# Kernel optimization log

Measured on AMD Instinct MI355X. Metric: run time of the kernel, lower is better.

The kernel has to match this reference:

```python
import jax, jax.numpy as jnp
import numpy as np

N, E = 50000, 800000
IN, EIN, HID, OUT = 128, 64, 256, 256
L, H = 3, 4
D = HID // H  # per-head out_feats


def setup_inputs() -> dict:
    key = jax.random.key(0)
    ks = jax.random.split(key, 20)
    s = 0.02
    return {
        "h": jax.random.normal(ks[0], (N, IN), jnp.float32),
        "efeat": jax.random.normal(ks[1], (E, EIN), jnp.float32),
        "src": jax.random.randint(ks[2], (E,), 0, N, jnp.int32),
        "dst": jax.random.randint(ks[3], (E,), 0, N, jnp.int32),
        "enc_w": jax.random.normal(ks[4], (IN, HID), jnp.float32) * s,
        "enc_b": jnp.zeros((HID,), jnp.float32),
        "eenc_w": jax.random.normal(ks[5], (EIN, HID), jnp.float32) * s,
        "eenc_b": jnp.zeros((HID,), jnp.float32),
        "Wn": jax.random.normal(ks[6], (L, HID, HID), jnp.float32) * s,
        "We": jax.random.normal(ks[7], (L, HID, HID), jnp.float32) * s,
        "al": jax.random.normal(ks[8], (L, H, D), jnp.float32) * s,
        "ar": jax.random.normal(ks[9], (L, H, D), jnp.float32) * s,
        "ae": jax.random.normal(ks[10], (L, H, D), jnp.float32) * s,
        "ln_g": jnp.ones((L, HID), jnp.float32),
        "ln_b": jnp.zeros((L, HID), jnp.float32),
        "out_w": jax.random.normal(ks[11], (HID, OUT), jnp.float32) * s,
        "out_b": jnp.zeros((OUT,), jnp.float32),
    }


def reference(h, efeat, src, dst, enc_w, enc_b, eenc_w, eenc_b,
              Wn, We, al, ar, ae, ln_g, ln_b, out_w, out_b):
    # Dropout layers act as identity (eval mode).
    n = h.shape[0]
    x = h @ enc_w + enc_b                      # [N, HID] node encoder
    ef = efeat @ eenc_w + eenc_b               # [E, HID] edge encoder
    nl, nh, nd = al.shape
    for l in range(nl):
        res = x
        feat = (x @ Wn[l]).reshape(n, nh, nd)          # [N,H,D]
        eft = (ef @ We[l]).reshape(-1, nh, nd)         # [E,H,D]
        el = jnp.sum(feat * al[l], axis=-1)            # [N,H]
        er = jnp.sum(feat * ar[l], axis=-1)            # [N,H]
        ee = jnp.sum(eft * ae[l], axis=-1)             # [E,H]
        e = jax.nn.leaky_relu(el[src] + er[dst] + ee, 0.2)  # [E,H]
        # edge softmax over incoming edges of each dst node
        m = jax.lax.stop_gradient(jax.ops.segment_max(e, dst, num_segments=n))
        a = jnp.exp(e - m[dst])
        ssum = jax.ops.segment_sum(a, dst, num_segments=n)
        alpha = a / ssum[dst]                          # [E,H]
        agg = jax.ops.segment_sum(alpha[:, :, None] * feat[src], dst,
                                  num_segments=n)      # [N,H,D]
        x = jax.nn.relu(agg.reshape(n, nh * nd))
        y = x + res
        mu = jnp.mean(y, axis=-1, keepdims=True)
        var = jnp.var(y, axis=-1, keepdims=True)
        x = (y - mu) / jnp.sqrt(var + 1e-5) * ln_g[l] + ln_b[l]
    return x @ out_w + out_b
```

## Files before the change

### kernel.cpp

```cpp
#include <hip/hip_runtime.h>
#include <math.h>


typedef __attribute__((ext_vector_type(8))) short bf16x8;
typedef __attribute__((ext_vector_type(4))) float f32x4;

__device__ __forceinline__ ushort f2b(float f) {
    unsigned u; __builtin_memcpy(&u, &f, 4);
    unsigned r = u + 0x7FFF + ((u >> 16) & 1);
    return (ushort)(r >> 16);
}
__device__ __forceinline__ float b2f(ushort u) {
    unsigned x = (unsigned)u << 16;
    float f; __builtin_memcpy(&f, &x, 4);
    return f;
}

__global__ void k_deg(const int* __restrict__ dst, int* __restrict__ deg, int E) {
    int e = blockIdx.x * 256 + threadIdx.x;
    if (e < E) atomicAdd(&deg[dst[e]], 1);
}

__global__ void k_bsum(const int* __restrict__ deg, int* __restrict__ bsum, int n) {
    __shared__ int wsum[4];
    int tid = threadIdx.x;
    int idx = blockIdx.x * 1024 + tid * 4;
    int4 v = make_int4(0, 0, 0, 0);
    if (idx + 3 < n) v = *(const int4*)(deg + idx);
    else {
        if (idx + 0 < n) v.x = deg[idx + 0];
        if (idx + 1 < n) v.y = deg[idx + 1];
        if (idx + 2 < n) v.z = deg[idx + 2];
    }
    int s = v.x + v.y + v.z + v.w;
#pragma unroll
    for (int off = 32; off; off >>= 1) s += __shfl_down(s, off, 64);
    if ((tid & 63) == 0) wsum[tid >> 6] = s;
    __syncthreads();
    if (tid == 0) bsum[blockIdx.x] = wsum[0] + wsum[1] + wsum[2] + wsum[3];
}

__global__ void k_bscan(const int* __restrict__ bsum, int* __restrict__ boff,
                        int* __restrict__ rowp, int NB, int n) {
    int tid = threadIdx.x;
    int v = (tid < NB) ? bsum[tid] : 0;
    int sc = v;
#pragma unroll
    for (int off = 1; off < 64; off <<= 1) {
        int t = __shfl_up(sc, off, 64);
        if ((tid & 63) >= off) sc += t;
    }
    if (tid < NB) boff[tid] = sc - v;
    if (tid == 63) rowp[n] = sc;
}

__global__ void k_bwrite(const int* __restrict__ deg, const int* __restrict__ boff,
                         int* __restrict__ rowp, int* __restrict__ cursor, int n) {
    __shared__ int wsum[4];
    __shared__ int woff_sh[4];
    int tid = threadIdx.x;
    int lane = tid & 63, wid = tid >> 6;
    int idx = blockIdx.x * 1024 + tid * 4;
    int4 v = make_int4(0, 0, 0, 0);
    if (idx + 3 < n) v = *(const int4*)(deg + idx);
    else {
        if (idx + 0 < n) v.x = deg[idx + 0];
        if (idx + 1 < n) v.y = deg[idx + 1];
        if (idx + 2 < n) v.z = deg[idx + 2];
    }
    int sum4 = v.x + v.y + v.z + v.w;
    int sc = sum4;
#pragma unroll
    for (int off = 1; off < 64; off <<= 1) {
        int t = __shfl_up(sc, off, 64);
        if (lane >= off) sc += t;
    }
    if (lane == 63) wsum[wid] = sc;
    __syncthreads();
    if (tid < 4) {
        int o = 0;
        for (int w = 0; w < tid; w++) o += wsum[w];
        woff_sh[tid] = o;
    }
    __syncthreads();
    int ex = boff[blockIdx.x] + woff_sh[wid] + (sc - sum4);
    int p0 = ex, p1 = ex + v.x, p2 = p1 + v.y, p3 = p2 + v.z;
    if (idx + 0 < n) { rowp[idx + 0] = p0; cursor[idx + 0] = p0; }
    if (idx + 1 < n) { rowp[idx + 1] = p1; cursor[idx + 1] = p1; }
    if (idx + 2 < n) { rowp[idx + 2] = p2; cursor[idx + 2] = p2; }
    if (idx + 3 < n) { rowp[idx + 3] = p3; cursor[idx + 3] = p3; }
}

__global__ void k_scatter(const int* __restrict__ dst, const int* __restrict__ src,
                          int* __restrict__ cursor, int* __restrict__ eid,
                          int* __restrict__ esrc, int E) {
    int e = blockIdx.x * 256 + threadIdx.x;
    if (e < E) {
        int pos = atomicAdd(&cursor[dst[e]], 1);
        eid[pos] = e;
        esrc[pos] = src[e];
    }
}

__global__ void k_ew(const float* __restrict__ We, const float* __restrict__ ae,
                     float* __restrict__ ew) {
    int t = blockIdx.x * 256 + threadIdx.x;
    if (t >= 3072) return;
    int l = t >> 10, r = t & 1023;
    int k = r >> 2, h = r & 3;
    const float* w = We + (size_t)l * 65536 + (size_t)k * 256 + h * 64;
    const float* a = ae + l * 256 + h * 64;
    float s = 0.f;
    for (int d = 0; d < 64; d++) s += w[d] * a[d];
    ew[t] = s;
}

__global__ void k_eew(const float* __restrict__ eenc_w, const float* __restrict__ eenc_b,
                      const float* __restrict__ ew, float* __restrict__ eew2,
                      float* __restrict__ eeb) {
    int t = blockIdx.x * 256 + threadIdx.x;
    if (t < 768) {
        int j = t / 12, lh = t % 12;
        int l = lh >> 2, h = lh & 3;
        float s = 0.f;
        for (int k = 0; k < 256; k++) s += eenc_w[j * 256 + k] * ew[l * 1024 + k * 4 + h];
        eew2[j * 12 + lh] = s;
    } else if (t < 780) {
        int lh = t - 768;
        int l = lh >> 2, h = lh & 3;
        float s = 0.f;
        for (int k = 0; k < 256; k++) s += eenc_b[k] * ew[l * 1024 + k * 4 + h];
        eeb[lh] = s;
    }
}

__global__ __launch_bounds__(256) void k_ee(const float* __restrict__ efeat,
                                            const float* __restrict__ eew2,
                                            const float* __restrict__ eeb,
                                            const int* __restrict__ eid,
                                            float* __restrict__ ee_l,
                                            int E) {
    const int tid = threadIdx.x;
    const int lane = tid & 63;
    const int wave = tid >> 6;
    const int q = lane & 7;
    const int g8 = lane >> 3;

    float W[8][12];
#pragma unroll
    for (int u = 0; u < 4; u++)
#pragma unroll
        for (int t = 0; t < 12; t++) {
            W[u][t]     = eew2[(q * 4 + u) * 12 + t];
            W[u + 4][t] = eew2[(32 + q * 4 + u) * 12 + t];
        }
    float Bv[12];
#pragma unroll
    for (int t = 0; t < 12; t++) Bv[t] = eeb[t];

    const int base = blockIdx.x * 128 + wave * 32;
#pragma unroll
    for (int p = 0; p < 4; p++) {
        int pos = base + p * 8 + g8;
        if (pos >= E) return;
        int e = eid[pos];
        float4 v0 = *(const float4*)(efeat + (size_t)e * 64 + q * 4);
        float4 v1 = *(const float4*)(efeat + (size_t)e * 64 + 32 + q * 4);
        float acc[12];
#pragma unroll
        for (int t = 0; t < 12; t++)
            acc[t] = v0.x * W[0][t] + v0.y * W[1][t] + v0.z * W[2][t] + v0.w * W[3][t] +
                     v1.x * W[4][t] + v1.y * W[5][t] + v1.z * W[6][t] + v1.w * W[7][t];
#pragma unroll
        for (int m = 1; m < 8; m <<= 1)
#pragma unroll
            for (int t = 0; t < 12; t++) acc[t] += __shfl_xor(acc[t], m, 64);
        if (q == 0) {
#pragma unroll
            for (int l = 0; l < 3; l++) {
                float4 o = make_float4(acc[l * 4 + 0] + Bv[l * 4 + 0],
                                       acc[l * 4 + 1] + Bv[l * 4 + 1],
                                       acc[l * 4 + 2] + Bv[l * 4 + 2],
                                       acc[l * 4 + 3] + Bv[l * 4 + 3]);
                *(float4*)(ee_l + (size_t)l * E * 4 + (size_t)pos * 4) = o;
            }
        }
    }
}

__global__ void k_prep(const float* __restrict__ h, const float* __restrict__ enc_w,
                       const float* __restrict__ Wn, const float* __restrict__ out_w,
                       ushort* __restrict__ hb, ushort* __restrict__ encT,
                       ushort* __restrict__ WnT, ushort* __restrict__ outT, int n4) {
    int t = blockIdx.x * 256 + threadIdx.x;
    if (t < n4) {
        float4 v = *(const float4*)(h + (size_t)t * 4);
        ushort4 o;
        o.x = f2b(v.x); o.y = f2b(v.y); o.z = f2b(v.z); o.w = f2b(v.w);
        *(ushort4*)(hb + (size_t)t * 4) = o;
        return;
    }
    t -= n4;
    if (t < 32768) {
        int nn = t >> 7, k = t & 127;
        encT[t] = f2b(enc_w[k * 256 + nn]);
        return;
    }
    t -= 32768;
    if (t < 3 * 65536) {
        int l = t >> 16, r = t & 65535;
        int nn = r >> 8, k = r & 255;
        WnT[(size_t)l * 65536 + r] = f2b(Wn[(size_t)l * 65536 + k * 256 + nn]);
        return;
    }
    t -= 3 * 65536;
    if (t < 65536) {
        int nn = t >> 8, k = t & 255;
        outT[t] = f2b(out_w[k * 256 + nn]);
    }
}

template <int KTILES, bool BIAS, bool STORE_F32, bool STORE_BF16>
__global__ __launch_bounds__(256) void gemm_mfma(const ushort* __restrict__ A,
                                                 const ushort* __restrict__ BT,
                                                 const float* __restrict__ bias,
                                                 float* __restrict__ Cf,
                                                 ushort* __restrict__ Cb, int M) {
    constexpr int K = KTILES * 32;
    __shared__ __align__(16) ushort As[128 * 32];
    __shared__ __align__(16) ushort Bs[128 * 32];
    const int tid = threadIdx.x;
    const int wave = tid >> 6;
    const int lane = tid & 63;
    const int rowBase = blockIdx.x * 128;
    const int colBase = blockIdx.y * 128;
    const int sRow = lane >> 2;
    const int sCol = (lane & 3) * 8;
    const int c0 = wave * 2, c1 = wave * 2 + 1;

    const ushort* gA0 = A + (size_t)(rowBase + c0 * 16 + sRow) * K + sCol;
    const ushort* gA1 = A + (size_t)(rowBase + c1 * 16 + sRow) * K + sCol;
    const ushort* gB0 = BT + (size_t)(colBase + c0 * 16 + sRow) * K + sCol;
    const ushort* gB1 = BT + (size_t)(colBase + c1 * 16 + sRow) * K + sCol;
    ushort* lA0 = As + c0 * 512;
    ushort* lA1 = As + c1 * 512;
    ushort* lB0 = Bs + c0 * 512;
    ushort* lB1 = Bs + c1 * 512;

    f32x4 acc[4][4] = {};
    const int wr = (wave >> 1) * 64, wc = (wave & 1) * 64;
    const int ml = lane & 15, q = lane >> 4;

    for (int kt = 0; kt < KTILES; ++kt) {
        __builtin_amdgcn_global_load_lds(
            (const __attribute__((address_space(1))) unsigned*)(gA0 + kt * 32),
            (__attribute__((address_space(3))) unsigned*)lA0, 16, 0, 0);
        __builtin_amdgcn_global_load_lds(
            (const __attribute__((address_space(1))) unsigned*)(gA1 + kt * 32),
            (__attribute__((address_space(3))) unsigned*)lA1, 16, 0, 0);
        __builtin_amdgcn_global_load_lds(
            (const __attribute__((address_space(1))) unsigned*)(gB0 + kt * 32),
            (__attribute__((address_space(3))) unsigned*)lB0, 16, 0, 0);
        __builtin_amdgcn_global_load_lds(
            (const __attribute__((address_space(1))) unsigned*)(gB1 + kt * 32),
            (__attribute__((address_space(3))) unsigned*)lB1, 16, 0, 0);
        __syncthreads();
        bf16x8 af[4], bfr[4];
#pragma unroll
        for (int i = 0; i < 4; i++)
            af[i] = *(const bf16x8*)&As[(wr + i * 16 + ml) * 32 + q * 8];
#pragma unroll
        for (int j = 0; j < 4; j++)
            bfr[j] = *(const bf16x8*)&Bs[(wc + j * 16 + ml) * 32 + q * 8];
#pragma unroll
        for (int i = 0; i < 4; i++)
#pragma unroll
            for (int j = 0; j < 4; j++)
                acc[i][j] = __builtin_amdgcn_mfma_f32_16x16x32_bf16(af[i], bfr[j], acc[i][j],
                                                                    0, 0, 0);
        __syncthreads();
    }

#pragma unroll
    for (int j = 0; j < 4; j++) {
        const int col = colBase + wc + j * 16 + ml;
        const float bb = BIAS ? bias[col] : 0.f;
#pragma unroll
        for (int i = 0; i < 4; i++) {
#pragma unroll
            for (int r = 0; r < 4; r++) {
                const int row = rowBase + wr + i * 16 + q * 4 + r;
                if (row < M) {
                    float v = acc[i][j][r] + bb;
                    if (STORE_F32) Cf[(size_t)row * 256 + col] = v;
                    if (STORE_BF16) Cb[(size_t)row * 256 + col] = f2b(v);
                }
            }
        }
    }
}

__global__ __launch_bounds__(256) void k_elr(const ushort* __restrict__ feat,
                                             const float* __restrict__ al,
                                             const float* __restrict__ ar,
                                             float* __restrict__ el,
                                             float* __restrict__ er, int N) {
    int lane = threadIdx.x & 63;
    int n = blockIdx.x * 4 + (threadIdx.x >> 6);
    if (n >= N) return;
    ushort4 f4 = *(const ushort4*)&feat[(size_t)n * 256 + lane * 4];
    float4 a4 = *(const float4*)&al[lane * 4];
    float4 r4 = *(const float4*)&ar[lane * 4];
    float f0 = b2f(f4.x), f1 = b2f(f4.y), f2 = b2f(f4.z), f3 = b2f(f4.w);
    float va = f0 * a4.x + f1 * a4.y + f2 * a4.z + f3 * a4.w;
    float vr = f0 * r4.x + f1 * r4.y + f2 * r4.z + f3 * r4.w;
#pragma unroll
    for (int m = 1; m < 16; m <<= 1) {
        va += __shfl_xor(va, m, 64);
        vr += __shfl_xor(vr, m, 64);
    }
    if ((lane & 15) == 0) {
        int h = lane >> 4;
        el[n * 4 + h] = va;
        er[n * 4 + h] = vr;
    }
}

template <bool WRITE_X>
__global__ __launch_bounds__(256) void k_agg(const int* __restrict__ rowp,
                                             const int* __restrict__ esrc,
                                             const float* __restrict__ ee,
                                             const float* __restrict__ el,
                                             const float* __restrict__ er,
                                             const ushort* __restrict__ feat,
                                             float* __restrict__ x_io,
                                             ushort* __restrict__ xb,
                                             const float* __restrict__ g,
                                             const float* __restrict__ b, int N) {
    __shared__ float w_sh[4][64][4];
    __shared__ int s_sh[4][64];
    const int wv = threadIdx.x >> 6;
    const int lane = threadIdx.x & 63;
    const int n = blockIdx.x * 4 + wv;
    if (n >= N) return;
    const int start = rowp[n], end = rowp[n + 1];
    const int h = lane >> 4;

    float4 e4 = *(const float4*)(er + (size_t)n * 4);
    float ern[4] = {e4.x, e4.y, e4.z, e4.w};
    float wsum[4] = {0.f, 0.f, 0.f, 0.f};
    float acc[4] = {0.f, 0.f, 0.f, 0.f};

    for (int cs = start; cs < end; cs += 64) {
        const int m = min(64, end - cs);
        if (lane < m) {
            int pos = cs + lane;
            int s = esrc[pos];
            s_sh[wv][lane] = s;
            float4 eev = *(const float4*)(ee + (size_t)pos * 4);
            float4 elv = *(const float4*)(el + (size_t)s * 4);
            float ea[4] = {eev.x, eev.y, eev.z, eev.w};
            float la[4] = {elv.x, elv.y, elv.z, elv.w};
#pragma unroll
            for (int hh = 0; hh < 4; hh++) {
                float sc = la[hh] + ern[hh] + ea[hh];
                sc = (sc > 0.f) ? sc : 0.2f * sc;
                float w = __expf(sc);
                w_sh[wv][lane][hh] = w;
                wsum[hh] += w;
            }
        }
        asm volatile("s_waitcnt lgkmcnt(0)" ::: "memory");
        __builtin_amdgcn_sched_barrier(0);
        for (int j = 0; j < m; ++j) {
            int s = s_sh[wv][j];
            float w = w_sh[wv][j][h];
            ushort4 p = *(const ushort4*)&feat[(size_t)s * 256 + lane * 4];
            acc[0] += w * b2f(p.x);
            acc[1] += w * b2f(p.y);
            acc[2] += w * b2f(p.z);
            acc[3] += w * b2f(p.w);
        }
        asm volatile("s_waitcnt lgkmcnt(0)" ::: "memory");
        __builtin_amdgcn_sched_barrier(0);
    }

#pragma unroll
    for (int mm = 1; mm < 64; mm <<= 1)
#pragma unroll
        for (int hh = 0; hh < 4; hh++) wsum[hh] += __shfl_xor(wsum[hh], mm, 64);

    float inv = (end > start) ? 1.f / wsum[h] : 0.f;
    float4 xr = *(const float4*)&x_io[(size_t)n * 256 + lane * 4];
    float xra[4] = {xr.x, xr.y, xr.z, xr.w};
    float y[4];
    float s1 = 0.f, s2 = 0.f;
#pragma unroll
    for (int u = 0; u < 4; u++) {
        float v = fmaxf(acc[u] * inv, 0.f);
        y[u] = v + xra[u];
        s1 += y[u];
        s2 += y[u] * y[u];
    }
#pragma unroll
    for (int mm = 1; mm < 64; mm <<= 1) {
        s1 += __shfl_xor(s1, mm, 64);
        s2 += __shfl_xor(s2, mm, 64);
    }
    float mu = s1 * (1.f / 256.f);
    float var = s2 * (1.f / 256.f) - mu * mu;
    float rstd = rsqrtf(var + 1e-5f);
    float4 gv = *(const float4*)&g[lane * 4];
    float4 bv = *(const float4*)&b[lane * 4];
    float ga[4] = {gv.x, gv.y, gv.z, gv.w};
    float ba[4] = {bv.x, bv.y, bv.z, bv.w};
    float o[4];
    ushort4 ob;
#pragma unroll
    for (int u = 0; u < 4; u++) o[u] = (y[u] - mu) * rstd * ga[u] + ba[u];
    ob.x = f2b(o[0]); ob.y = f2b(o[1]); ob.z = f2b(o[2]); ob.w = f2b(o[3]);
    if (WRITE_X)
        *(float4*)&x_io[(size_t)n * 256 + lane * 4] = make_float4(o[0], o[1], o[2], o[3]);
    *(ushort4*)&xb[(size_t)n * 256 + lane * 4] = ob;
}

extern "C" void kernel_launch(void* const* d_in, const int* in_sizes, int n_in,
                              void* d_out, int out_size, void* d_ws, size_t ws_size,
                              hipStream_t stream) {
    const float* h      = (const float*)d_in[0];
    const float* efeat  = (const float*)d_in[1];
    const int*   src    = (const int*)d_in[2];
    const int*   dst    = (const int*)d_in[3];
    const float* enc_w  = (const float*)d_in[4];
    const float* enc_b  = (const float*)d_in[5];
    const float* eenc_w = (const float*)d_in[6];
    const float* eenc_b = (const float*)d_in[7];
    const float* Wn     = (const float*)d_in[8];
    const float* We     = (const float*)d_in[9];
    const float* al     = (const float*)d_in[10];
    const float* ar     = (const float*)d_in[11];
    const float* ae     = (const float*)d_in[12];
    const float* ln_g   = (const float*)d_in[13];
    const float* ln_b   = (const float*)d_in[14];
    const float* out_w  = (const float*)d_in[15];
    const float* out_b  = (const float*)d_in[16];

    const int N = in_sizes[0] / 128;
    const int E = in_sizes[2];
    const int Mpad = ((N + 127) / 128) * 128;
    const int NB = (N + 1023) / 1024;

    char* ws = (char*)d_ws;
    size_t off = 0;
    auto alloc = [&](size_t bytes) -> char* {
        char* p = ws + off;
        off += (bytes + 255) & ~(size_t)255;
        return p;
    };
    float*  X      = (float*)alloc((size_t)Mpad * 256 * 4);
    ushort* Xb     = (ushort*)alloc((size_t)Mpad * 256 * 2);
    ushort* F      = (ushort*)alloc((size_t)Mpad * 256 * 2);
    ushort* hb     = (ushort*)alloc((size_t)Mpad * 128 * 2);
    float*  el     = (float*)alloc((size_t)N * 4 * 4);
    float*  er     = (float*)alloc((size_t)N * 4 * 4);
    float*  ee_l   = (float*)alloc((size_t)E * 12 * 4);
    int*    esrc   = (int*)alloc((size_t)E * 4);
    int*    eid    = (int*)alloc((size_t)E * 4);
    int*    deg    = (int*)alloc((size_t)N * 4);
    int*    rowp   = (int*)alloc((size_t)(N + 1) * 4);
    int*    cursor = (int*)alloc((size_t)N * 4);
    int*    bsum   = (int*)alloc(64 * 4);
    int*    boff   = (int*)alloc(64 * 4);
    float*  ew     = (float*)alloc(3072 * 4);
    float*  eew2   = (float*)alloc(768 * 4);
    float*  eeb    = (float*)alloc(64);
    ushort* encT   = (ushort*)alloc(256 * 128 * 2);
    ushort* WnT    = (ushort*)alloc(3 * 256 * 256 * 2);
    ushort* outT   = (ushort*)alloc(256 * 256 * 2);
    (void)ws_size; (void)n_in; (void)out_size;

    hipMemsetAsync(deg, 0, (size_t)N * 4, stream);
    k_deg<<<(E + 255) / 256, 256, 0, stream>>>(dst, deg, E);
    k_bsum<<<NB, 256, 0, stream>>>(deg, bsum, N);
    k_bscan<<<1, 64, 0, stream>>>(bsum, boff, rowp, NB, N);
    k_bwrite<<<NB, 256, 0, stream>>>(deg, boff, rowp, cursor, N);
    k_scatter<<<(E + 255) / 256, 256, 0, stream>>>(dst, src, cursor, eid, esrc, E);

    k_ew<<<12, 256, 0, stream>>>(We, ae, ew);
    k_eew<<<4, 256, 0, stream>>>(eenc_w, eenc_b, ew, eew2, eeb);
    k_ee<<<(E + 127) / 128, 256, 0, stream>>>(efeat, eew2, eeb, eid, ee_l, E);

    const int n4 = N * 128 / 4;
    k_prep<<<(n4 + 32768 + 4 * 65536 + 255) / 256, 256, 0, stream>>>(
        h, enc_w, Wn, out_w, hb, encT, WnT, outT, n4);

    dim3 gG(Mpad / 128, 2);
    gemm_mfma<4, true, true, true><<<gG, 256, 0, stream>>>(hb, encT, enc_b, X, Xb, N);

    for (int l = 0; l < 3; l++) {
        gemm_mfma<8, false, false, true><<<gG, 256, 0, stream>>>(
            Xb, WnT + (size_t)l * 65536, nullptr, nullptr, F, N);
        k_elr<<<(N + 3) / 4, 256, 0, stream>>>(F, al + l * 256, ar + l * 256, el, er, N);
        if (l < 2)
            k_agg<true><<<(N + 3) / 4, 256, 0, stream>>>(rowp, esrc,
                ee_l + (size_t)l * E * 4, el, er, F, X, Xb, ln_g + l * 256,
                ln_b + l * 256, N);
        else
            k_agg<false><<<(N + 3) / 4, 256, 0, stream>>>(rowp, esrc,
                ee_l + (size_t)l * E * 4, el, er, F, X, Xb, ln_g + l * 256,
                ln_b + l * 256, N);
    }
    gemm_mfma<8, true, true, false><<<gG, 256, 0, stream>>>(Xb, outT, out_b,
                                                            (float*)d_out, nullptr, N);
}
```

Measured before the change: 862.5 us.

## Split edge gather across wave halves with 16-byte loads; drop fp32 residual copy

The aggregation kernel now has each half-wave process alternate edges and each lane load 8 bf16 features (16 bytes) instead of 4, combining the halves with a cross-half shuffle. The fp32 node-state buffer X is removed, so the residual is read from the bf16 copy Xb and only bf16 is written back. This cuts per-node global traffic and doubles in-flight gathers per lane. The residual path now carries bf16 rounding instead of fp32 precision, which may shift accuracy slightly.

```diff
diff --git a/kernel.cpp b/kernel.cpp
--- a/kernel.cpp
+++ b/kernel.cpp
@@ -3,6 +3,7 @@
 
 
 typedef __attribute__((ext_vector_type(8))) short bf16x8;
+typedef __attribute__((ext_vector_type(8))) unsigned short u16x8;
 typedef __attribute__((ext_vector_type(4))) float f32x4;
 
 __device__ __forceinline__ ushort f2b(float f) {
@@ -326,14 +327,12 @@
     }
 }
 
-template <bool WRITE_X>
 __global__ __launch_bounds__(256) void k_agg(const int* __restrict__ rowp,
                                              const int* __restrict__ esrc,
                                              const float* __restrict__ ee,
                                              const float* __restrict__ el,
                                              const float* __restrict__ er,
                                              const ushort* __restrict__ feat,
-                                             float* __restrict__ x_io,
                                              ushort* __restrict__ xb,
                                              const float* __restrict__ g,
                                              const float* __restrict__ b, int N) {
@@ -344,12 +343,14 @@
     const int n = blockIdx.x * 4 + wv;
     if (n >= N) return;
     const int start = rowp[n], end = rowp[n + 1];
-    const int h = lane >> 4;
+    const int half = lane >> 5;
+    const int c = lane & 31;
+    const int h = c >> 3;
 
     float4 e4 = *(const float4*)(er + (size_t)n * 4);
     float ern[4] = {e4.x, e4.y, e4.z, e4.w};
     float wsum[4] = {0.f, 0.f, 0.f, 0.f};
-    float acc[4] = {0.f, 0.f, 0.f, 0.f};
+    float acc[8] = {0.f, 0.f, 0.f, 0.f, 0.f, 0.f, 0.f, 0.f};
 
     for (int cs = start; cs < end; cs += 64) {
         const int m = min(64, end - cs);
@@ -372,33 +373,33 @@
         }
         asm volatile("s_waitcnt lgkmcnt(0)" ::: "memory");
         __builtin_amdgcn_sched_barrier(0);
-        for (int j = 0; j < m; ++j) {
+        for (int j = half; j < m; j += 2) {
             int s = s_sh[wv][j];
             float w = w_sh[wv][j][h];
-            ushort4 p = *(const ushort4*)&feat[(size_t)s * 256 + lane * 4];
-            acc[0] += w * b2f(p.x);
-            acc[1] += w * b2f(p.y);
-            acc[2] += w * b2f(p.z);
-            acc[3] += w * b2f(p.w);
+            u16x8 p = *(const u16x8*)&feat[(size_t)s * 256 + c * 8];
+#pragma unroll
+            for (int u = 0; u < 8; u++) acc[u] += w * b2f((ushort)p[u]);
         }
         asm volatile("s_waitcnt lgkmcnt(0)" ::: "memory");
         __builtin_amdgcn_sched_barrier(0);
     }
 
 #pragma unroll
+    for (int u = 0; u < 8; u++) acc[u] += __shfl_xor(acc[u], 32, 64);
+
+#pragma unroll
     for (int mm = 1; mm < 64; mm <<= 1)
 #pragma unroll
         for (int hh = 0; hh < 4; hh++) wsum[hh] += __shfl_xor(wsum[hh], mm, 64);
 
     float inv = (end > start) ? 1.f / wsum[h] : 0.f;
-    float4 xr = *(const float4*)&x_io[(size_t)n * 256 + lane * 4];
-    float xra[4] = {xr.x, xr.y, xr.z, xr.w};
-    float y[4];
+    u16x8 xr = *(const u16x8*)&xb[(size_t)n * 256 + c * 8];
+    float y[8];
     float s1 = 0.f, s2 = 0.f;
 #pragma unroll
-    for (int u = 0; u < 4; u++) {
+    for (int u = 0; u < 8; u++) {
         float v = fmaxf(acc[u] * inv, 0.f);
-        y[u] = v + xra[u];
+        y[u] = v + b2f((ushort)xr[u]);
         s1 += y[u];
         s2 += y[u] * y[u];
     }
@@ -407,21 +408,20 @@
         s1 += __shfl_xor(s1, mm, 64);
         s2 += __shfl_xor(s2, mm, 64);
     }
-    float mu = s1 * (1.f / 256.f);
-    float var = s2 * (1.f / 256.f) - mu * mu;
+    float mu = s1 * (1.f / 512.f);
+    float var = s2 * (1.f / 512.f) - mu * mu;
     float rstd = rsqrtf(var + 1e-5f);
-    float4 gv = *(const float4*)&g[lane * 4];
-    float4 bv = *(const float4*)&b[lane * 4];
-    float ga[4] = {gv.x, gv.y, gv.z, gv.w};
-    float ba[4] = {bv.x, bv.y, bv.z, bv.w};
-    float o[4];
-    ushort4 ob;
-#pragma unroll
-    for (int u = 0; u < 4; u++) o[u] = (y[u] - mu) * rstd * ga[u] + ba[u];
-    ob.x = f2b(o[0]); ob.y = f2b(o[1]); ob.z = f2b(o[2]); ob.w = f2b(o[3]);
-    if (WRITE_X)
-        *(float4*)&x_io[(size_t)n * 256 + lane * 4] = make_float4(o[0], o[1], o[2], o[3]);
-    *(ushort4*)&xb[(size_t)n * 256 + lane * 4] = ob;
+    float4 gv0 = *(const float4*)&g[c * 8];
+    float4 gv1 = *(const float4*)&g[c * 8 + 4];
+    float4 bv0 = *(const float4*)&b[c * 8];
+    float4 bv1 = *(const float4*)&b[c * 8 + 4];
+    float ga[8] = {gv0.x, gv0.y, gv0.z, gv0.w, gv1.x, gv1.y, gv1.z, gv1.w};
+    float ba[8] = {bv0.x, bv0.y, bv0.z, bv0.w, bv1.x, bv1.y, bv1.z, bv1.w};
+    u16x8 ob;
+#pragma unroll
+    for (int u = 0; u < 8; u++) ob[u] = f2b((y[u] - mu) * rstd * ga[u] + ba[u]);
+    if (half == 0)
+        *(u16x8*)&xb[(size_t)n * 256 + c * 8] = ob;
 }
 
 extern "C" void kernel_launch(void* const* d_in, const int* in_sizes, int n_in,
@@ -457,7 +457,6 @@
         off += (bytes + 255) & ~(size_t)255;
         return p;
     };
-    float*  X      = (float*)alloc((size_t)Mpad * 256 * 4);
     ushort* Xb     = (ushort*)alloc((size_t)Mpad * 256 * 2);
     ushort* F      = (ushort*)alloc((size_t)Mpad * 256 * 2);
     ushort* hb     = (ushort*)alloc((size_t)Mpad * 128 * 2);
@@ -495,20 +494,16 @@
         h, enc_w, Wn, out_w, hb, encT, WnT, outT, n4);
 
     dim3 gG(Mpad / 128, 2);
-    gemm_mfma<4, true, true, true><<<gG, 256, 0, stream>>>(hb, encT, enc_b, X, Xb, N);
+    gemm_mfma<4, true, false, true><<<gG, 256, 0, stream>>>(hb, encT, enc_b,
+                                                            nullptr, Xb, N);
 
     for (int l = 0; l < 3; l++) {
         gemm_mfma<8, false, false, true><<<gG, 256, 0, stream>>>(
             Xb, WnT + (size_t)l * 65536, nullptr, nullptr, F, N);
         k_elr<<<(N + 3) / 4, 256, 0, stream>>>(F, al + l * 256, ar + l * 256, el, er, N);
-        if (l < 2)
-            k_agg<true><<<(N + 3) / 4, 256, 0, stream>>>(rowp, esrc,
-                ee_l + (size_t)l * E * 4, el, er, F, X, Xb, ln_g + l * 256,
-                ln_b + l * 256, N);
-        else
-            k_agg<false><<<(N + 3) / 4, 256, 0, stream>>>(rowp, esrc,
-                ee_l + (size_t)l * E * 4, el, er, F, X, Xb, ln_g + l * 256,
-                ln_b + l * 256, N);
+        k_agg<<<(N + 3) / 4, 256, 0, stream>>>(rowp, esrc, ee_l + (size_t)l * E * 4,
+                                               el, er, F, Xb, ln_g + l * 256,
+                                               ln_b + l * 256, N);
     }
     gemm_mfma<8, true, true, false><<<gG, 256, 0, stream>>>(Xb, outT, out_b,
                                                             (float*)d_out, nullptr, N);
```

After: 829.9 us. 1.04x faster.
